# Optimization experiments

Hardware: AMD Instinct MI355X
Metric: run time of the kernel (lower is better)

Reference implementation:

```python
import jax, jax.numpy as jnp
import numpy as np

EPS = 1e-8
LN_EPS = 1e-5
PSCALE = 10.0
P = 8  # n_points


def _bb_frames(Xn, Xca, Xc):
    # Gram-Schmidt rigid frame from N, CA, C (AlphaFold rigids_from_3_points).
    v1 = Xc - Xca
    v2 = Xn - Xca
    e1 = v1 / jnp.sqrt(jnp.sum(v1 * v1, -1, keepdims=True) + EPS)
    u2 = v2 - e1 * jnp.sum(e1 * v2, -1, keepdims=True)
    e2 = u2 / jnp.sqrt(jnp.sum(u2 * u2, -1, keepdims=True) + EPS)
    e3 = jnp.cross(e1, e2)
    R = jnp.stack([e1, e2, e3], axis=-1)  # [B,N,3,3], columns are basis vectors
    t = Xca / PSCALE                      # scale_translation(1/position_scale)
    return R, t


def _layernorm(x, g, b):
    mu = jnp.mean(x, -1, keepdims=True)
    var = jnp.mean((x - mu) ** 2, -1, keepdims=True)
    return (x - mu) / jnp.sqrt(var + LN_EPS) * g + b


def setup_inputs() -> dict:
    key = jax.random.key(0)
    ks = jax.random.split(key, 24)
    B, N, K, D, H = 8, 512, 32, 128, 128
    msg_in = 2 * D + D + 9 * P  # 456
    s = 0.02
    inp = {
        "h_V": jax.random.normal(ks[0], (B, N, D), jnp.float32),
        "h_E": jax.random.normal(ks[1], (B, N, K, D), jnp.float32),
        "X": jax.random.normal(ks[2], (B, N, 3, 3), jnp.float32),
        "mask_V": jnp.ones((B, N), jnp.float32),
        "mask_attend": jnp.ones((B, N, K), jnp.float32),
        "Wp": jax.random.normal(ks[3], (D, P * 3), jnp.float32) * s,
        "bp": jnp.zeros((P * 3,), jnp.float32),
        "Wm1": jax.random.normal(ks[4], (msg_in, H), jnp.float32) * s,
        "bm1": jnp.zeros((H,), jnp.float32),
        "Wm2": jax.random.normal(ks[5], (H, H), jnp.float32) * s,
        "bm2": jnp.zeros((H,), jnp.float32),
        "Wm3": jax.random.normal(ks[6], (H, H), jnp.float32) * s,
        "bm3": jnp.zeros((H,), jnp.float32),
        "g1": jnp.ones((H,), jnp.float32),
        "be1": jnp.zeros((H,), jnp.float32),
        "Wd1": jax.random.normal(ks[7], (H, 4 * H), jnp.float32) * s,
        "bd1": jnp.zeros((4 * H,), jnp.float32),
        "Wd2": jax.random.normal(ks[8], (4 * H, H), jnp.float32) * s,
        "bd2": jnp.zeros((H,), jnp.float32),
        "g2": jnp.ones((H,), jnp.float32),
        "be2": jnp.zeros((H,), jnp.float32),
        "E_idx": jax.random.randint(ks[9], (B, N, K), 0, N, jnp.int32),
    }
    return inp


def reference(h_V, h_E, X, mask_V, mask_attend,
              Wp, bp, Wm1, bm1, Wm2, bm2, Wm3, bm3, g1, be1,
              Wd1, bd1, Wd2, bd2, g2, be2, E_idx):
    B, N, K = E_idx.shape
    R, t = _bb_frames(X[..., 0, :], X[..., 1, :], X[..., 2, :])
    # local points [B,N,P,3]
    p_local = (h_V @ Wp + bp).reshape(B, N, P, 3)
    # global points: R @ p + t
    p_global = jnp.einsum('bnij,bnpj->bnpi', R, p_local) + t[:, :, None, :]
    bidx = jnp.arange(B)[:, None, None]
    nbr_pg = p_global[bidx, E_idx]  # [B,N,K,P,3]
    nbr_hV = h_V[bidx, E_idx]       # [B,N,K,D]
    # distances in global frame
    diff = p_global[:, :, None] - nbr_pg
    npg_norm = jnp.sqrt(jnp.sum(diff * diff, -1) + EPS)  # [B,N,K,P]
    # neighbor points in local frame: R^T (q - t)
    q = nbr_pg - t[:, :, None, None, :]
    nbr_pl = jnp.einsum('bnij,bnkpi->bnkpj', R, q)       # [B,N,K,P,3]
    npl_norm = jnp.sqrt(jnp.sum(nbr_pl * nbr_pl, -1) + EPS)
    pl_norm = jnp.sqrt(jnp.sum(p_local * p_local, -1) + EPS)  # [B,N,P]

    D = h_V.shape[-1]
    node_expand = jnp.broadcast_to(h_V[:, :, None, :], (B, N, K, D))
    pl_flat = jnp.broadcast_to(p_local[:, :, None], (B, N, K, P, 3)).reshape(B, N, K, P * 3)
    pl_norm_e = jnp.broadcast_to(pl_norm[:, :, None, :], (B, N, K, P))
    msg_in = jnp.concatenate([
        node_expand, h_E, nbr_hV,
        pl_flat, pl_norm_e,
        nbr_pl.reshape(B, N, K, P * 3), npl_norm, npg_norm,
    ], axis=-1)

    # node_message_fn: 3-layer MLP with relu
    m = jax.nn.relu(msg_in @ Wm1 + bm1)
    m = jax.nn.relu(m @ Wm2 + bm2)
    m = m @ Wm3 + bm3
    m = m * mask_attend[..., None]
    node_m = jnp.mean(m, axis=-2)  # [B,N,H]

    h = _layernorm(h_V + node_m, g1, be1)  # dropout = identity (eval)
    dense = jax.nn.relu(h @ Wd1 + bd1) @ Wd2 + bd2
    h = _layernorm(h + dense, g2, be2)
    h = h * mask_V[..., None]
    return h, h_E
```

## Files before the change

### kernel.cpp

```cpp
#include <hip/hip_runtime.h>
#include <hip/hip_bf16.h>

typedef __hip_bfloat16 bf16;
typedef __attribute__((ext_vector_type(8))) short s16x8;
typedef __attribute__((ext_vector_type(4))) float f32x4;

#define DEV __device__ __forceinline__

DEV float us2f(unsigned short u){ return __uint_as_float(((unsigned int)u) << 16); }
DEV unsigned short f2us(float f){
    __hip_bfloat16 h = __float2bfloat16(f);
    unsigned short r; __builtin_memcpy(&r, &h, 2); return r;
}
DEV unsigned pack2(float a, float b){ return (unsigned)f2us(a) | ((unsigned)f2us(b) << 16); }

template<bool F32> DEV float ldf(const void* p, long i){
    if (F32) return reinterpret_cast<const float*>(p)[i];
    return us2f(reinterpret_cast<const unsigned short*>(p)[i]);
}
template<bool F32> DEV unsigned short ld16(const void* p, long i){
    if (F32) return f2us(reinterpret_cast<const float*>(p)[i]);
    return reinterpret_cast<const unsigned short*>(p)[i];
}

union U16x8 { uint4 u; s16x8 v; };

DEV bool is_f32(const void* maskV){
    return reinterpret_cast<const unsigned short*>(maskV)[0] != 0x3F80;
}

template<bool F32>
DEV void wtrans_body(const void* Wm1, const void* Wm2, const void* Wm3,
                     const void* Wp, const void* Wd1, const void* Wd2,
                     unsigned short* wt1, unsigned short* wt2, unsigned short* wt3,
                     unsigned short* wpT, unsigned short* wd1T, unsigned short* wd2T,
                     long t)
{
    if (t < 61440) {
        int k = (int)(t >> 7), h = (int)(t & 127);
        wt1[(long)h*480 + k] = (k < 456) ? ld16<F32>(Wm1, (long)k*128 + h) : (unsigned short)0;
    } else if (t < 77824) {
        long t2 = t - 61440; int k = (int)(t2 >> 7), h = (int)(t2 & 127);
        wt2[(long)h*128 + k] = ld16<F32>(Wm2, (long)k*128 + h);
    } else if (t < 94208) {
        long t2 = t - 77824; int k = (int)(t2 >> 7), h = (int)(t2 & 127);
        wt3[(long)h*128 + k] = ld16<F32>(Wm3, (long)k*128 + h);
    } else if (t < 97280) {
        long t2 = t - 94208; int i = (int)(t2 / 24), j = (int)(t2 % 24);
        wpT[(long)j*128 + i] = ld16<F32>(Wp, (long)i*24 + j);
    } else if (t < 162816) {
        long t2 = t - 97280; int k = (int)(t2 >> 9), n = (int)(t2 & 511);
        wd1T[(long)n*128 + k] = ld16<F32>(Wd1, (long)k*512 + n);
    } else if (t < 228352) {
        long t2 = t - 162816; int k = (int)(t2 >> 7), n = (int)(t2 & 127);
        wd2T[(long)n*512 + k] = ld16<F32>(Wd2, (long)k*128 + n);
    }
}

__global__ __launch_bounds__(256) void wtrans_k(
    const void* __restrict__ Wm1, const void* __restrict__ Wm2, const void* __restrict__ Wm3,
    const void* __restrict__ Wp, const void* __restrict__ Wd1, const void* __restrict__ Wd2,
    unsigned short* __restrict__ wt1, unsigned short* __restrict__ wt2,
    unsigned short* __restrict__ wt3, unsigned short* __restrict__ wpT,
    unsigned short* __restrict__ wd1T, unsigned short* __restrict__ wd2T,
    const void* __restrict__ maskV)
{
    long t = (long)blockIdx.x*256 + threadIdx.x;
    if (is_f32(maskV)) wtrans_body<true >(Wm1,Wm2,Wm3,Wp,Wd1,Wd2,wt1,wt2,wt3,wpT,wd1T,wd2T,t);
    else               wtrans_body<false>(Wm1,Wm2,Wm3,Wp,Wd1,Wd2,wt1,wt2,wt3,wpT,wd1T,wd2T,t);
}

struct PrepSmem { float sX[9], sR[9], st[3], spl[24], hvs[128]; };

template<bool F32>
DEV void prep_body(const void* hV, const void* X, const unsigned short* wpT, const void* bp,
                   float* pg, float* pl, float* pln, float* Rw, float* tw,
                   PrepSmem& s, int n, int tid)
{
    if (tid < 9) s.sX[tid] = ldf<F32>(X, (long)n*9 + tid);
    for (int i = tid; i < 128; i += 64) s.hvs[i] = ldf<F32>(hV, (long)n*128 + i);
    __syncthreads();

    if (tid == 0) {
        float Nx=s.sX[0],Ny=s.sX[1],Nz=s.sX[2];
        float Ax=s.sX[3],Ay=s.sX[4],Az=s.sX[5];
        float Cx=s.sX[6],Cy=s.sX[7],Cz=s.sX[8];
        float v1x=Cx-Ax, v1y=Cy-Ay, v1z=Cz-Az;
        float v2x=Nx-Ax, v2y=Ny-Ay, v2z=Nz-Az;
        float r1 = 1.f/sqrtf(v1x*v1x+v1y*v1y+v1z*v1z + 1e-8f);
        float e1x=v1x*r1, e1y=v1y*r1, e1z=v1z*r1;
        float dp = e1x*v2x+e1y*v2y+e1z*v2z;
        float u2x=v2x-e1x*dp, u2y=v2y-e1y*dp, u2z=v2z-e1z*dp;
        float r2 = 1.f/sqrtf(u2x*u2x+u2y*u2y+u2z*u2z + 1e-8f);
        float e2x=u2x*r2, e2y=u2y*r2, e2z=u2z*r2;
        float e3x = e1y*e2z - e1z*e2y;
        float e3y = e1z*e2x - e1x*e2z;
        float e3z = e1x*e2y - e1y*e2x;
        s.sR[0]=e1x; s.sR[1]=e2x; s.sR[2]=e3x;
        s.sR[3]=e1y; s.sR[4]=e2y; s.sR[5]=e3y;
        s.sR[6]=e1z; s.sR[7]=e2z; s.sR[8]=e3z;
        s.st[0]=Ax*0.1f; s.st[1]=Ay*0.1f; s.st[2]=Az*0.1f;
    }
    if (tid < 24) {
        float acc = ldf<F32>(bp, tid);
        const unsigned short* wr = wpT + (long)tid*128;
        #pragma unroll
        for (int c=0;c<16;c++){
            ushort4 w0 = *reinterpret_cast<const ushort4*>(wr + c*8);
            ushort4 w1 = *reinterpret_cast<const ushort4*>(wr + c*8 + 4);
            acc += s.hvs[c*8+0]*us2f(w0.x) + s.hvs[c*8+1]*us2f(w0.y)
                 + s.hvs[c*8+2]*us2f(w0.z) + s.hvs[c*8+3]*us2f(w0.w)
                 + s.hvs[c*8+4]*us2f(w1.x) + s.hvs[c*8+5]*us2f(w1.y)
                 + s.hvs[c*8+6]*us2f(w1.z) + s.hvs[c*8+7]*us2f(w1.w);
        }
        s.spl[tid] = acc;
    }
    __syncthreads();

    if (tid < 24) {
        pl[n*24+tid] = s.spl[tid];
        int p = tid/3, c = tid - p*3;
        float g = s.sR[c*3+0]*s.spl[p*3+0] + s.sR[c*3+1]*s.spl[p*3+1]
                + s.sR[c*3+2]*s.spl[p*3+2] + s.st[c];
        pg[n*24+tid] = g;
    }
    if (tid < 9) Rw[n*9+tid] = s.sR[tid];
    if (tid < 3) tw[n*3+tid] = s.st[tid];
    if (tid < 8) {
        float a=s.spl[tid*3], b=s.spl[tid*3+1], c=s.spl[tid*3+2];
        pln[n*8+tid] = sqrtf(a*a+b*b+c*c + 1e-8f);
    }
}

__global__ __launch_bounds__(64) void prep_k(
    const void* __restrict__ hV, const void* __restrict__ X,
    const unsigned short* __restrict__ wpT, const void* __restrict__ bp,
    float* __restrict__ pg, float* __restrict__ pl, float* __restrict__ pln,
    float* __restrict__ Rw, float* __restrict__ tw, const void* __restrict__ maskV)
{
    __shared__ PrepSmem s;
    int n = blockIdx.x, tid = threadIdx.x;
    if (is_f32(maskV)) prep_body<true >(hV,X,wpT,bp,pg,pl,pln,Rw,tw,s,n,tid);
    else               prep_body<false>(hV,X,wpT,bp,pg,pl,pln,Rw,tw,s,n,tid);
}

#define ASTRIDE 40
#define MSTRIDE 136

struct __align__(16) Mp1Smem {
    union __align__(16) {
        unsigned short geo[3][64*ASTRIDE];
        unsigned short m[64*MSTRIDE];
    } u;
    int   sj[64];
    float smka[64];
    float spg[2][24], spl[2][24], spln[2][8], sR[2][9], st3[2][3];
};

template<bool F32>
DEV void mpnn1_body(
    const void* hV, const void* hE, const void* maskA,
    const void* bm1, const void* bm2, const void* bm3, const int* Eidx,
    const float* pg, const float* pl, const float* pln,
    const float* Rw, const float* tw,
    const unsigned short* wt1, const unsigned short* wt2, const unsigned short* wt3,
    float* nodemsg, void* outE, Mp1Smem& sm, int n0, int tid)
{
    const int lane = tid & 63, w = tid >> 6;
    const int lm = lane & 15, quad = lane >> 4;

    if (tid < 64) { int l = tid >> 5;
        sm.sj[tid] = (((n0+l) >> 9) << 9) + Eidx[(long)(n0+l)*32 + (tid & 31)];
    } else { int t = tid - 64; int l = t >> 5;
        sm.smka[t] = ldf<F32>(maskA, (long)(n0+l)*32 + (t & 31));
    }
    if (tid < 48)        { sm.spg[tid/24][tid%24] = pg[(n0+tid/24)*24 + tid%24]; }
    else if (tid < 96)   { int t=tid-48; sm.spl[t/24][t%24] = pl[(n0+t/24)*24 + t%24]; }
    else if (tid < 112)  { int t=tid-96; sm.spln[t>>3][t&7]  = pln[(n0+(t>>3))*8 + (t&7)]; }
    if (tid < 18)        { sm.sR[tid/9][tid%9] = Rw[(n0+tid/9)*9 + tid%9]; }
    else if (tid < 24)   { int t=tid-18; sm.st3[t/3][t%3] = tw[(n0+t/3)*3 + t%3]; }
    __syncthreads();

    #pragma unroll
    for (int pass=0; pass<4; ++pass) {
        int v = tid + pass*128;
        int row = v >> 3, p = v & 7, nd = row >> 5;
        int j = sm.sj[row];
        float qx = pg[j*24 + p*3 + 0];
        float qy = pg[j*24 + p*3 + 1];
        float qz = pg[j*24 + p*3 + 2];
        float dx = sm.spg[nd][p*3+0]-qx, dy = sm.spg[nd][p*3+1]-qy, dz = sm.spg[nd][p*3+2]-qz;
        float npg = sqrtf(dx*dx+dy*dy+dz*dz + 1e-8f);
        float ux = qx - sm.st3[nd][0], uy = qy - sm.st3[nd][1], uz = qz - sm.st3[nd][2];
        float l0 = sm.sR[nd][0]*ux + sm.sR[nd][3]*uy + sm.sR[nd][6]*uz;
        float l1 = sm.sR[nd][1]*ux + sm.sR[nd][4]*uy + sm.sR[nd][7]*uz;
        float l2v= sm.sR[nd][2]*ux + sm.sR[nd][5]*uy + sm.sR[nd][8]*uz;
        float npl = sqrtf(l0*l0+l1*l1+l2v*l2v + 1e-8f);
        unsigned short* C0 = sm.u.geo[0];
        unsigned short* C1 = sm.u.geo[1];
        unsigned short* C2 = sm.u.geo[2];
        C0[row*ASTRIDE + p*3+0] = f2us(sm.spl[nd][p*3+0]);
        C0[row*ASTRIDE + p*3+1] = f2us(sm.spl[nd][p*3+1]);
        C0[row*ASTRIDE + p*3+2] = f2us(sm.spl[nd][p*3+2]);
        C0[row*ASTRIDE + 24+p]  = f2us(sm.spln[nd][p]);
        C1[row*ASTRIDE + p*3+0] = f2us(l0);
        C1[row*ASTRIDE + p*3+1] = f2us(l1);
        C1[row*ASTRIDE + p*3+2] = f2us(l2v);
        C1[row*ASTRIDE + 24+p]  = f2us(npl);
        C2[row*ASTRIDE + p]     = f2us(npg);
    }
    for (int z = tid; z < 64*24; z += 128) {
        int row = z / 24, col = 8 + (z % 24);
        sm.u.geo[2][row*ASTRIDE + col] = 0;
    }
    __syncthreads();

    int sjv[4];
    #pragma unroll
    for (int mt=0; mt<4; ++mt) sjv[mt] = sm.sj[16*mt + lm];

    const unsigned short* wr1[4];
    #pragma unroll
    for (int nt=0; nt<4; ++nt) wr1[nt] = wt1 + (long)(64*w + nt*16 + lm)*480 + quad*8;

    f32x4 acc[4][4];
    #pragma unroll
    for (int nt=0; nt<4; ++nt) {
        float b0 = ldf<F32>(bm1, 64*w + nt*16 + lm);
        f32x4 iv = {b0,b0,b0,b0};
        #pragma unroll
        for (int mt=0; mt<4; ++mt) acc[mt][nt] = iv;
    }

    for (int c=0; c<15; ++c) {
        s16x8 av[4];
        if (c < 12) {
            #pragma unroll
            for (int mt=0; mt<4; ++mt) {
                int row16 = 16*mt + lm, nd = mt >> 1;
                const void* base; long src;
                if (c < 4)      { base = hV; src = (long)(n0+nd)*128 + c*32 + quad*8; }
                else if (c < 8) { base = hE; src = ((long)(n0+nd)*32 + (row16&31))*128 + (c-4)*32 + quad*8; }
                else            { base = hV; src = (long)sjv[mt]*128 + (c-8)*32 + quad*8; }
                U16x8 pk;
                if (F32) {
                    const float4* vp = reinterpret_cast<const float4*>(reinterpret_cast<const float*>(base) + src);
                    float4 x = vp[0], y = vp[1];
                    if (c >= 4 && c < 8 && w == 0) {
                        float4* d = reinterpret_cast<float4*>(reinterpret_cast<float*>(outE) + src);
                        d[0] = x; d[1] = y;
                    }
                    pk.u.x = pack2(x.x,x.y); pk.u.y = pack2(x.z,x.w);
                    pk.u.z = pack2(y.x,y.y); pk.u.w = pack2(y.z,y.w);
                } else {
                    pk.u = *reinterpret_cast<const uint4*>(reinterpret_cast<const unsigned short*>(base) + src);
                    if (c >= 4 && c < 8 && w == 0)
                        *reinterpret_cast<uint4*>(reinterpret_cast<unsigned short*>(outE) + src) = pk.u;
                }
                av[mt] = pk.v;
            }
        } else {
            #pragma unroll
            for (int mt=0; mt<4; ++mt)
                av[mt] = *reinterpret_cast<const s16x8*>(&sm.u.geo[c-12][(16*mt+lm)*ASTRIDE + quad*8]);
        }
        #pragma unroll
        for (int nt=0; nt<4; ++nt) {
            s16x8 bf = *reinterpret_cast<const s16x8*>(wr1[nt] + (long)c*32);
            #pragma unroll
            for (int mt=0; mt<4; ++mt)
                acc[mt][nt] = __builtin_amdgcn_mfma_f32_16x16x32_bf16(av[mt], bf, acc[mt][nt], 0,0,0);
        }
    }
    __syncthreads();

    #pragma unroll
    for (int mt=0; mt<4; ++mt)
        #pragma unroll
        for (int nt=0; nt<4; ++nt)
            #pragma unroll
            for (int r=0; r<4; ++r)
                sm.u.m[(16*mt + quad*4 + r)*MSTRIDE + 64*w + nt*16 + lm]
                    = f2us(fmaxf(acc[mt][nt][r], 0.f));
    __syncthreads();

    #pragma unroll
    for (int nt=0; nt<4; ++nt) {
        float b0 = ldf<F32>(bm2, 64*w + nt*16 + lm);
        f32x4 iv = {b0,b0,b0,b0};
        #pragma unroll
        for (int mt=0; mt<4; ++mt) acc[mt][nt] = iv;
    }
    #pragma unroll
    for (int kc=0; kc<4; ++kc) {
        s16x8 av[4];
        #pragma unroll
        for (int mt=0; mt<4; ++mt)
            av[mt] = *reinterpret_cast<const s16x8*>(&sm.u.m[(16*mt+lm)*MSTRIDE + kc*32 + quad*8]);
        #pragma unroll
        for (int nt=0; nt<4; ++nt) {
            s16x8 bf = *reinterpret_cast<const s16x8*>(&wt2[(long)(64*w + nt*16 + lm)*128 + kc*32 + quad*8]);
            #pragma unroll
            for (int mt=0; mt<4; ++mt)
                acc[mt][nt] = __builtin_amdgcn_mfma_f32_16x16x32_bf16(av[mt], bf, acc[mt][nt], 0,0,0);
        }
    }
    __syncthreads();

    #pragma unroll
    for (int mt=0; mt<4; ++mt)
        #pragma unroll
        for (int nt=0; nt<4; ++nt)
            #pragma unroll
            for (int r=0; r<4; ++r)
                sm.u.m[(16*mt + quad*4 + r)*MSTRIDE + 64*w + nt*16 + lm]
                    = f2us(fmaxf(acc[mt][nt][r], 0.f));
    __syncthreads();

    #pragma unroll
    for (int nt=0; nt<4; ++nt) {
        float b0 = ldf<F32>(bm3, 64*w + nt*16 + lm);
        f32x4 iv = {b0,b0,b0,b0};
        #pragma unroll
        for (int mt=0; mt<4; ++mt) acc[mt][nt] = iv;
    }
    #pragma unroll
    for (int kc=0; kc<4; ++kc) {
        s16x8 av[4];
        #pragma unroll
        for (int mt=0; mt<4; ++mt)
            av[mt] = *reinterpret_cast<const s16x8*>(&sm.u.m[(16*mt+lm)*MSTRIDE + kc*32 + quad*8]);
        #pragma unroll
        for (int nt=0; nt<4; ++nt) {
            s16x8 bf = *reinterpret_cast<const s16x8*>(&wt3[(long)(64*w + nt*16 + lm)*128 + kc*32 + quad*8]);
            #pragma unroll
            for (int mt=0; mt<4; ++mt)
                acc[mt][nt] = __builtin_amdgcn_mfma_f32_16x16x32_bf16(av[mt], bf, acc[mt][nt], 0,0,0);
        }
    }

    #pragma unroll
    for (int nt=0; nt<4; ++nt) {
        float s0 = 0.f, s1 = 0.f;
        #pragma unroll
        for (int r=0; r<4; ++r) {
            s0 += acc[0][nt][r] * sm.smka[     quad*4 + r]
                + acc[1][nt][r] * sm.smka[16 + quad*4 + r];
            s1 += acc[2][nt][r] * sm.smka[32 + quad*4 + r]
                + acc[3][nt][r] * sm.smka[48 + quad*4 + r];
        }
        s0 += __shfl_xor(s0, 16); s0 += __shfl_xor(s0, 32);
        s1 += __shfl_xor(s1, 16); s1 += __shfl_xor(s1, 32);
        if (lane < 16) {
            nodemsg[(long)(n0  )*128 + 64*w + nt*16 + lane] = s0;
            nodemsg[(long)(n0+1)*128 + 64*w + nt*16 + lane] = s1;
        }
    }
}

__global__ __launch_bounds__(128) void mpnn1_k(
    const void* __restrict__ hV, const void* __restrict__ hE,
    const void* __restrict__ maskV, const void* __restrict__ maskA,
    const void* __restrict__ bm1, const void* __restrict__ bm2, const void* __restrict__ bm3,
    const int* __restrict__ Eidx,
    const float* __restrict__ pg, const float* __restrict__ pl,
    const float* __restrict__ pln, const float* __restrict__ Rw,
    const float* __restrict__ tw,
    const unsigned short* __restrict__ wt1, const unsigned short* __restrict__ wt2,
    const unsigned short* __restrict__ wt3,
    float* __restrict__ nodemsg, void* __restrict__ dout)
{
    __shared__ Mp1Smem sm;
    int n0 = blockIdx.x * 2, tid = threadIdx.x;
    if (is_f32(maskV)) {
        void* outE = reinterpret_cast<float*>(dout) + 524288;
        mpnn1_body<true >(hV,hE,maskA,bm1,bm2,bm3,Eidx,pg,pl,pln,Rw,tw,wt1,wt2,wt3,nodemsg,outE,sm,n0,tid);
    } else {
        void* outE = reinterpret_cast<unsigned short*>(dout) + 524288;
        mpnn1_body<false>(hV,hE,maskA,bm1,bm2,bm3,Eidx,pg,pl,pln,Rw,tw,wt1,wt2,wt3,nodemsg,outE,sm,n0,tid);
    }
}

#define TSTRIDE 520

struct __align__(16) FfnSmem {
    unsigned short x1[32*MSTRIDE];
    union __align__(16) {
        unsigned short t1[32*TSTRIDE];
        float yf[32*132];
    } u;
};

template<bool F32>
DEV void ffn_body(const void* hV, const void* maskV, const float* nodemsg,
                  const void* g1, const void* be1, const void* bd1, const void* bd2,
                  const void* g2, const void* be2,
                  const unsigned short* wd1T, const unsigned short* wd2T,
                  void* out, FfnSmem& sm, int n0, int tid)
{
    const int lane = tid & 63, w = tid >> 6;
    const int mt = w >> 1, h = w & 1;
    const int lm = lane & 15, quad = lane >> 4;

    {
        const int r = tid >> 3, c0 = (tid & 7) * 16;
        const long nb = (long)(n0 + r)*128;
        float xv[16];
        float s1 = 0.f, s2 = 0.f;
        #pragma unroll
        for (int j=0; j<16; ++j) {
            float v = ldf<F32>(hV, nb + c0 + j) + nodemsg[nb + c0 + j] * (1.f/32.f);
            xv[j] = v; s1 += v; s2 += v*v;
        }
        s1 += __shfl_xor(s1,1); s1 += __shfl_xor(s1,2); s1 += __shfl_xor(s1,4);
        s2 += __shfl_xor(s2,1); s2 += __shfl_xor(s2,2); s2 += __shfl_xor(s2,4);
        float mu = s1 * (1.f/128.f);
        float var = s2 * (1.f/128.f) - mu*mu;
        float rs = 1.f/sqrtf(var + 1e-5f);
        #pragma unroll
        for (int j=0; j<16; ++j) {
            int c = c0 + j;
            sm.x1[r*MSTRIDE + c] = f2us((xv[j]-mu)*rs*ldf<F32>(g1, c) + ldf<F32>(be1, c));
        }
    }
    __syncthreads();

    {
        f32x4 t1a[16];
        #pragma unroll
        for (int nt=0; nt<16; ++nt) {
            float b0 = ldf<F32>(bd1, 256*h + nt*16 + lm);
            f32x4 iv = {b0,b0,b0,b0};
            t1a[nt] = iv;
        }
        #pragma unroll
        for (int kc=0; kc<4; ++kc) {
            s16x8 a = *reinterpret_cast<const s16x8*>(&sm.x1[(16*mt+lm)*MSTRIDE + kc*32 + quad*8]);
            #pragma unroll
            for (int nt=0; nt<16; ++nt) {
                s16x8 bf = *reinterpret_cast<const s16x8*>(&wd1T[(long)(256*h + nt*16 + lm)*128 + kc*32 + quad*8]);
                t1a[nt] = __builtin_amdgcn_mfma_f32_16x16x32_bf16(a, bf, t1a[nt], 0,0,0);
            }
        }
        #pragma unroll
        for (int nt=0; nt<16; ++nt)
            #pragma unroll
            for (int r=0; r<4; ++r)
                sm.u.t1[(16*mt + quad*4 + r)*TSTRIDE + 256*h + nt*16 + lm] = f2us(fmaxf(t1a[nt][r], 0.f));
    }
    __syncthreads();

    f32x4 yacc[4];
    #pragma unroll
    for (int nt=0; nt<4; ++nt) {
        float b0 = ldf<F32>(bd2, 64*h + nt*16 + lm);
        f32x4 iv = {b0,b0,b0,b0};
        yacc[nt] = iv;
    }
    #pragma unroll
    for (int kc=0; kc<16; ++kc) {
        s16x8 a = *reinterpret_cast<const s16x8*>(&sm.u.t1[(16*mt+lm)*TSTRIDE + kc*32 + quad*8]);
        #pragma unroll
        for (int nt=0; nt<4; ++nt) {
            s16x8 bf = *reinterpret_cast<const s16x8*>(&wd2T[(long)(64*h + nt*16 + lm)*512 + kc*32 + quad*8]);
            yacc[nt] = __builtin_amdgcn_mfma_f32_16x16x32_bf16(a, bf, yacc[nt], 0,0,0);
        }
    }
    __syncthreads();

    #pragma unroll
    for (int nt=0; nt<4; ++nt)
        #pragma unroll
        for (int r=0; r<4; ++r) {
            int rr = 16*mt + quad*4 + r, c = 64*h + nt*16 + lm;
            sm.u.yf[rr*132 + c] = yacc[nt][r] + us2f(sm.x1[rr*MSTRIDE + c]);
        }
    __syncthreads();

    {
        const int r = tid >> 3, c0 = (tid & 7) * 16;
        float yv[16];
        float s1 = 0.f, s2 = 0.f;
        #pragma unroll
        for (int j=0; j<16; ++j) {
            float v = sm.u.yf[r*132 + c0 + j];
            yv[j] = v; s1 += v; s2 += v*v;
        }
        s1 += __shfl_xor(s1,1); s1 += __shfl_xor(s1,2); s1 += __shfl_xor(s1,4);
        s2 += __shfl_xor(s2,1); s2 += __shfl_xor(s2,2); s2 += __shfl_xor(s2,4);
        float mu = s1 * (1.f/128.f);
        float var = s2 * (1.f/128.f) - mu*mu;
        float rs = 1.f/sqrtf(var + 1e-5f);
        float mv = ldf<F32>(maskV, n0 + r);
        const long ob = (long)(n0 + r)*128 + c0;
        #pragma unroll
        for (int j=0; j<16; ++j) {
            int c = c0 + j;
            float v = ((yv[j]-mu)*rs*ldf<F32>(g2, c) + ldf<F32>(be2, c)) * mv;
            if (F32) reinterpret_cast<float*>(out)[ob + j] = v;
            else     reinterpret_cast<unsigned short*>(out)[ob + j] = f2us(v);
        }
    }
}

__global__ __launch_bounds__(256) void ffn_k(
    const void* __restrict__ hV, const void* __restrict__ maskV,
    const float* __restrict__ nodemsg,
    const void* __restrict__ g1, const void* __restrict__ be1,
    const void* __restrict__ bd1, const void* __restrict__ bd2,
    const void* __restrict__ g2, const void* __restrict__ be2,
    const unsigned short* __restrict__ wd1T, const unsigned short* __restrict__ wd2T,
    void* __restrict__ out)
{
    __shared__ FfnSmem sm;
    int n0 = blockIdx.x * 32, tid = threadIdx.x;
    if (is_f32(maskV))
        ffn_body<true >(hV,maskV,nodemsg,g1,be1,bd1,bd2,g2,be2,wd1T,wd2T,out,sm,n0,tid);
    else
        ffn_body<false>(hV,maskV,nodemsg,g1,be1,bd1,bd2,g2,be2,wd1T,wd2T,out,sm,n0,tid);
}

extern "C" void kernel_launch(void* const* d_in, const int* in_sizes, int n_in,
                              void* d_out, int out_size, void* d_ws, size_t ws_size,
                              hipStream_t stream)
{
    const void* hV    = d_in[0];
    const void* hE    = d_in[1];
    const void* X     = d_in[2];
    const void* maskV = d_in[3];
    const void* maskA = d_in[4];
    const void* Wp    = d_in[5];
    const void* bp    = d_in[6];
    const void* Wm1   = d_in[7];
    const void* bm1   = d_in[8];
    const void* Wm2   = d_in[9];
    const void* bm2   = d_in[10];
    const void* Wm3   = d_in[11];
    const void* bm3   = d_in[12];
    const void* g1    = d_in[13];
    const void* be1   = d_in[14];
    const void* Wd1   = d_in[15];
    const void* bd1   = d_in[16];
    const void* Wd2   = d_in[17];
    const void* bd2   = d_in[18];
    const void* g2    = d_in[19];
    const void* be2   = d_in[20];
    const int*  Eidx  = (const int*)d_in[21];

    float* ws = (float*)d_ws;
    float* pg  = ws;
    float* pl  = ws + 98304;
    float* pln = ws + 196608;
    float* Rw  = ws + 229376;
    float* tw  = ws + 266240;
    float* nm  = ws + 278528;
    unsigned short* wt1  = (unsigned short*)(ws + 802816);
    unsigned short* wt2  = wt1 + 61440;
    unsigned short* wt3  = wt2 + 16384;
    unsigned short* wpT  = wt3 + 16384;
    unsigned short* wd1T = wpT + 3072;
    unsigned short* wd2T = wd1T + 65536;

    wtrans_k<<<892, 256, 0, stream>>>(Wm1, Wm2, Wm3, Wp, Wd1, Wd2,
                                      wt1, wt2, wt3, wpT, wd1T, wd2T, maskV);

    prep_k<<<4096, 64, 0, stream>>>(hV, X, wpT, bp, pg, pl, pln, Rw, tw, maskV);

    mpnn1_k<<<2048, 128, 0, stream>>>(hV, hE, maskV, maskA, bm1, bm2, bm3, Eidx,
                                      pg, pl, pln, Rw, tw, wt1, wt2, wt3,
                                      nm, d_out);

    ffn_k<<<128, 256, 0, stream>>>(hV, maskV, nm, g1, be1, bd1, bd2, g2, be2,
                                   wd1T, wd2T, d_out);
}
```

Baseline: 277.6 us.

## Precompute per-node first-layer projections of node and neighbor features

Splits the first message-MLP layer by linearity: the node-feature and neighbor-feature parts are projected once per node (U = hV·W_self + b, V = hV·W_nbr) in a new small kernel. The edge kernel then gathers the projected V rows by neighbor index and adds U and V before the ReLU. This removes 8 of 15 K-chunks of MFMA work and the raw neighbor-feature gathers per edge. In exchange it adds a kernel launch, workspace traffic for U/V, and extra register pressure from the 64 gathered fp32 values per thread. The projections are added in fp32 rather than taken from bf16 inputs, which slightly changes rounding.

```diff
diff --git a/kernel.cpp b/kernel.cpp
--- a/kernel.cpp
+++ b/kernel.cpp
@@ -68,6 +68,64 @@
     long t = (long)blockIdx.x*256 + threadIdx.x;
     if (is_f32(maskV)) wtrans_body<true >(Wm1,Wm2,Wm3,Wp,Wd1,Wd2,wt1,wt2,wt3,wpT,wd1T,wd2T,t);
     else               wtrans_body<false>(Wm1,Wm2,Wm3,Wp,Wd1,Wd2,wt1,wt2,wt3,wpT,wd1T,wd2T,t);
+}
+
+template<bool F32>
+DEV void uv_body(const void* hV, const void* bm1, const unsigned short* wt1,
+                 float* Uw, float* Vw, int r0, int tid)
+{
+    const int lane = tid & 63, w = tid >> 6;
+    const int lm = lane & 15, quad = lane >> 4;
+
+    s16x8 af[4];
+    #pragma unroll
+    for (int kc=0; kc<4; ++kc) {
+        long src = (long)(r0 + lm)*128 + kc*32 + quad*8;
+        U16x8 pk;
+        if (F32) {
+            const float4* vp = reinterpret_cast<const float4*>(reinterpret_cast<const float*>(hV) + src);
+            float4 x = vp[0], y = vp[1];
+            pk.u.x = pack2(x.x,x.y); pk.u.y = pack2(x.z,x.w);
+            pk.u.z = pack2(y.x,y.y); pk.u.w = pack2(y.z,y.w);
+        } else {
+            pk.u = *reinterpret_cast<const uint4*>(reinterpret_cast<const unsigned short*>(hV) + src);
+        }
+        af[kc] = pk.v;
+    }
+
+    const int koff = w ? 256 : 0;
+    f32x4 acc[8];
+    #pragma unroll
+    for (int nt=0; nt<8; ++nt) {
+        float b0 = w ? 0.f : ldf<F32>(bm1, nt*16 + lm);
+        f32x4 iv = {b0,b0,b0,b0};
+        acc[nt] = iv;
+    }
+    #pragma unroll
+    for (int kc=0; kc<4; ++kc) {
+        #pragma unroll
+        for (int nt=0; nt<8; ++nt) {
+            s16x8 bf = *reinterpret_cast<const s16x8*>(wt1 + (long)(nt*16 + lm)*480 + koff + kc*32 + quad*8);
+            acc[nt] = __builtin_amdgcn_mfma_f32_16x16x32_bf16(af[kc], bf, acc[nt], 0,0,0);
+        }
+    }
+    float* out = w ? Vw : Uw;
+    #pragma unroll
+    for (int nt=0; nt<8; ++nt)
+        #pragma unroll
+        for (int r=0; r<4; ++r)
+            out[(long)(r0 + quad*4 + r)*128 + nt*16 + lm] = acc[nt][r];
+}
+
+__global__ __launch_bounds__(128) void uv_k(
+    const void* __restrict__ hV, const void* __restrict__ bm1,
+    const unsigned short* __restrict__ wt1,
+    float* __restrict__ Uw, float* __restrict__ Vw,
+    const void* __restrict__ maskV)
+{
+    int r0 = blockIdx.x * 16, tid = threadIdx.x;
+    if (is_f32(maskV)) uv_body<true >(hV, bm1, wt1, Uw, Vw, r0, tid);
+    else               uv_body<false>(hV, bm1, wt1, Uw, Vw, r0, tid);
 }
 
 struct PrepSmem { float sX[9], sR[9], st[3], spl[24], hvs[128]; };
@@ -160,10 +218,11 @@
 template<bool F32>
 DEV void mpnn1_body(
     const void* hV, const void* hE, const void* maskA,
-    const void* bm1, const void* bm2, const void* bm3, const int* Eidx,
+    const void* bm2, const void* bm3, const int* Eidx,
     const float* pg, const float* pl, const float* pln,
     const float* Rw, const float* tw,
     const unsigned short* wt1, const unsigned short* wt2, const unsigned short* wt3,
+    const float* Uw, const float* Vw,
     float* nodemsg, void* outE, Mp1Smem& sm, int n0, int tid)
 {
     const int lane = tid & 63, w = tid >> 6;
@@ -180,6 +239,23 @@
     if (tid < 18)        { sm.sR[tid/9][tid%9] = Rw[(n0+tid/9)*9 + tid%9]; }
     else if (tid < 24)   { int t=tid-18; sm.st3[t/3][t%3] = tw[(n0+t/3)*3 + t%3]; }
     __syncthreads();
+
+    float vg[4][4][4];
+    float ug[2][4];
+    #pragma unroll
+    for (int mt=0; mt<4; ++mt)
+        #pragma unroll
+        for (int r=0; r<4; ++r) {
+            int j = sm.sj[16*mt + quad*4 + r];
+            #pragma unroll
+            for (int nt=0; nt<4; ++nt)
+                vg[mt][r][nt] = Vw[(long)j*128 + 64*w + nt*16 + lm];
+        }
+    #pragma unroll
+    for (int nd=0; nd<2; ++nd)
+        #pragma unroll
+        for (int nt=0; nt<4; ++nt)
+            ug[nd][nt] = Uw[(long)(n0+nd)*128 + 64*w + nt*16 + lm];
 
     #pragma unroll
     for (int pass=0; pass<4; ++pass) {
@@ -215,63 +291,65 @@
     }
     __syncthreads();
 
-    int sjv[4];
-    #pragma unroll
-    for (int mt=0; mt<4; ++mt) sjv[mt] = sm.sj[16*mt + lm];
-
     const unsigned short* wr1[4];
     #pragma unroll
     for (int nt=0; nt<4; ++nt) wr1[nt] = wt1 + (long)(64*w + nt*16 + lm)*480 + quad*8;
 
     f32x4 acc[4][4];
-    #pragma unroll
-    for (int nt=0; nt<4; ++nt) {
-        float b0 = ldf<F32>(bm1, 64*w + nt*16 + lm);
-        f32x4 iv = {b0,b0,b0,b0};
-        #pragma unroll
-        for (int mt=0; mt<4; ++mt) acc[mt][nt] = iv;
-    }
-
-    for (int c=0; c<15; ++c) {
+    {
+        f32x4 zv = {0.f,0.f,0.f,0.f};
+        #pragma unroll
+        for (int mt=0; mt<4; ++mt)
+            #pragma unroll
+            for (int nt=0; nt<4; ++nt) acc[mt][nt] = zv;
+    }
+
+    #pragma unroll
+    for (int c=0; c<4; ++c) {
         s16x8 av[4];
-        if (c < 12) {
-            #pragma unroll
-            for (int mt=0; mt<4; ++mt) {
-                int row16 = 16*mt + lm, nd = mt >> 1;
-                const void* base; long src;
-                if (c < 4)      { base = hV; src = (long)(n0+nd)*128 + c*32 + quad*8; }
-                else if (c < 8) { base = hE; src = ((long)(n0+nd)*32 + (row16&31))*128 + (c-4)*32 + quad*8; }
-                else            { base = hV; src = (long)sjv[mt]*128 + (c-8)*32 + quad*8; }
-                U16x8 pk;
-                if (F32) {
-                    const float4* vp = reinterpret_cast<const float4*>(reinterpret_cast<const float*>(base) + src);
-                    float4 x = vp[0], y = vp[1];
-                    if (c >= 4 && c < 8 && w == 0) {
-                        float4* d = reinterpret_cast<float4*>(reinterpret_cast<float*>(outE) + src);
-                        d[0] = x; d[1] = y;
-                    }
-                    pk.u.x = pack2(x.x,x.y); pk.u.y = pack2(x.z,x.w);
-                    pk.u.z = pack2(y.x,y.y); pk.u.w = pack2(y.z,y.w);
-                } else {
-                    pk.u = *reinterpret_cast<const uint4*>(reinterpret_cast<const unsigned short*>(base) + src);
-                    if (c >= 4 && c < 8 && w == 0)
-                        *reinterpret_cast<uint4*>(reinterpret_cast<unsigned short*>(outE) + src) = pk.u;
+        #pragma unroll
+        for (int mt=0; mt<4; ++mt) {
+            int row16 = 16*mt + lm, nd = mt >> 1;
+            long src = ((long)(n0+nd)*32 + (row16&31))*128 + c*32 + quad*8;
+            U16x8 pk;
+            if (F32) {
+                const float4* vp = reinterpret_cast<const float4*>(reinterpret_cast<const float*>(hE) + src);
+                float4 x = vp[0], y = vp[1];
+                if (w == 0) {
+                    float4* d = reinterpret_cast<float4*>(reinterpret_cast<float*>(outE) + src);
+                    d[0] = x; d[1] = y;
                 }
-                av[mt] = pk.v;
+                pk.u.x = pack2(x.x,x.y); pk.u.y = pack2(x.z,x.w);
+                pk.u.z = pack2(y.x,y.y); pk.u.w = pack2(y.z,y.w);
+            } else {
+                pk.u = *reinterpret_cast<const uint4*>(reinterpret_cast<const unsigned short*>(hE) + src);
+                if (w == 0)
+                    *reinterpret_cast<uint4*>(reinterpret_cast<unsigned short*>(outE) + src) = pk.u;
             }
-        } else {
-            #pragma unroll
-            for (int mt=0; mt<4; ++mt)
-                av[mt] = *reinterpret_cast<const s16x8*>(&sm.u.geo[c-12][(16*mt+lm)*ASTRIDE + quad*8]);
+            av[mt] = pk.v;
         }
         #pragma unroll
         for (int nt=0; nt<4; ++nt) {
-            s16x8 bf = *reinterpret_cast<const s16x8*>(wr1[nt] + (long)c*32);
+            s16x8 bf = *reinterpret_cast<const s16x8*>(wr1[nt] + (long)(c+4)*32);
             #pragma unroll
             for (int mt=0; mt<4; ++mt)
                 acc[mt][nt] = __builtin_amdgcn_mfma_f32_16x16x32_bf16(av[mt], bf, acc[mt][nt], 0,0,0);
         }
     }
+    #pragma unroll
+    for (int c=0; c<3; ++c) {
+        s16x8 av[4];
+        #pragma unroll
+        for (int mt=0; mt<4; ++mt)
+            av[mt] = *reinterpret_cast<const s16x8*>(&sm.u.geo[c][(16*mt+lm)*ASTRIDE + quad*8]);
+        #pragma unroll
+        for (int nt=0; nt<4; ++nt) {
+            s16x8 bf = *reinterpret_cast<const s16x8*>(wr1[nt] + (long)(c+12)*32);
+            #pragma unroll
+            for (int mt=0; mt<4; ++mt)
+                acc[mt][nt] = __builtin_amdgcn_mfma_f32_16x16x32_bf16(av[mt], bf, acc[mt][nt], 0,0,0);
+        }
+    }
     __syncthreads();
 
     #pragma unroll
@@ -281,7 +359,7 @@
             #pragma unroll
             for (int r=0; r<4; ++r)
                 sm.u.m[(16*mt + quad*4 + r)*MSTRIDE + 64*w + nt*16 + lm]
-                    = f2us(fmaxf(acc[mt][nt][r], 0.f));
+                    = f2us(fmaxf(acc[mt][nt][r] + ug[mt>>1][nt] + vg[mt][r][nt], 0.f));
     __syncthreads();
 
     #pragma unroll
@@ -361,23 +439,24 @@
 __global__ __launch_bounds__(128) void mpnn1_k(
     const void* __restrict__ hV, const void* __restrict__ hE,
     const void* __restrict__ maskV, const void* __restrict__ maskA,
-    const void* __restrict__ bm1, const void* __restrict__ bm2, const void* __restrict__ bm3,
+    const void* __restrict__ bm2, const void* __restrict__ bm3,
     const int* __restrict__ Eidx,
     const float* __restrict__ pg, const float* __restrict__ pl,
     const float* __restrict__ pln, const float* __restrict__ Rw,
     const float* __restrict__ tw,
     const unsigned short* __restrict__ wt1, const unsigned short* __restrict__ wt2,
     const unsigned short* __restrict__ wt3,
+    const float* __restrict__ Uw, const float* __restrict__ Vw,
     float* __restrict__ nodemsg, void* __restrict__ dout)
 {
     __shared__ Mp1Smem sm;
     int n0 = blockIdx.x * 2, tid = threadIdx.x;
     if (is_f32(maskV)) {
         void* outE = reinterpret_cast<float*>(dout) + 524288;
-        mpnn1_body<true >(hV,hE,maskA,bm1,bm2,bm3,Eidx,pg,pl,pln,Rw,tw,wt1,wt2,wt3,nodemsg,outE,sm,n0,tid);
+        mpnn1_body<true >(hV,hE,maskA,bm2,bm3,Eidx,pg,pl,pln,Rw,tw,wt1,wt2,wt3,Uw,Vw,nodemsg,outE,sm,n0,tid);
     } else {
         void* outE = reinterpret_cast<unsigned short*>(dout) + 524288;
-        mpnn1_body<false>(hV,hE,maskA,bm1,bm2,bm3,Eidx,pg,pl,pln,Rw,tw,wt1,wt2,wt3,nodemsg,outE,sm,n0,tid);
+        mpnn1_body<false>(hV,hE,maskA,bm2,bm3,Eidx,pg,pl,pln,Rw,tw,wt1,wt2,wt3,Uw,Vw,nodemsg,outE,sm,n0,tid);
     }
 }
 
@@ -560,15 +639,19 @@
     unsigned short* wpT  = wt3 + 16384;
     unsigned short* wd1T = wpT + 3072;
     unsigned short* wd2T = wd1T + 65536;
+    float* Uw = ws + 917504;
+    float* Vw = Uw + 524288;
 
     wtrans_k<<<892, 256, 0, stream>>>(Wm1, Wm2, Wm3, Wp, Wd1, Wd2,
                                       wt1, wt2, wt3, wpT, wd1T, wd2T, maskV);
 
+    uv_k<<<256, 128, 0, stream>>>(hV, bm1, wt1, Uw, Vw, maskV);
+
     prep_k<<<4096, 64, 0, stream>>>(hV, X, wpT, bp, pg, pl, pln, Rw, tw, maskV);
 
-    mpnn1_k<<<2048, 128, 0, stream>>>(hV, hE, maskV, maskA, bm1, bm2, bm3, Eidx,
+    mpnn1_k<<<2048, 128, 0, stream>>>(hV, hE, maskV, maskA, bm2, bm3, Eidx,
                                       pg, pl, pln, Rw, tw, wt1, wt2, wt3,
-                                      nm, d_out);
+                                      Uw, Vw, nm, d_out);
 
     ffn_k<<<128, 256, 0, stream>>>(hV, maskV, nm, g1, be1, bd1, bd2, g2, be2,
                                    wd1T, wd2T, d_out);
```

Result: faster. 269.9 us (-2.8%).
